# Performance work log

Measured on AMD Instinct MI355X. Metric: run time of the kernel, lower is better.

## Reference

```python
import jax, jax.numpy as jnp
import numpy as np

RADIUS = 4
SIGMA_X = 4.0
SIGMA_I = 10.0
P = 64                      # patch_size
NS = 2 * RADIUS + 1         # neighborhood_size = 9
EPS = float(np.finfo(np.float64).eps)


def _dist_weights():
    # Faithful to torch: dist varies only along the LAST window axis
    # (torch `expand` of a 1-D tensor to (9,9,9) broadcasts along dim -1).
    d = jnp.arange(1, NS + 1) - (RADIUS + 1)          # -4..4
    dist3d = jnp.broadcast_to(3 * d ** 2, (NS, NS, NS)).astype(jnp.float32)
    mask = (dist3d <= RADIUS).astype(jnp.float32)
    return (mask * jnp.exp(-dist3d / SIGMA_X ** 2)).reshape(-1)  # (729,)


_OFFSETS = jnp.asarray(
    np.stack(np.meshgrid(np.arange(NS), np.arange(NS), np.arange(NS), indexing='ij'),
             axis=-1).reshape(-1, 3), dtype=jnp.int32)            # (729, 3)


def _forward(batch, preds):
    B = batch.shape[0]
    K = preds.shape[1]
    pad = [(0, 0), (0, 0), (RADIUS, RADIUS), (RADIUS, RADIUS), (RADIUS, RADIUS)]
    pb = jnp.pad(batch, pad, constant_values=EPS)   # [B,1,P+2r,P+2r,P+2r]
    pp = jnp.pad(preds, pad, constant_values=EPS)   # [B,K,P+2r,P+2r,P+2r]
    dw = _dist_weights()

    def body(carry, od):
        off, w_o = od
        num, den = carry
        img_win = jax.lax.dynamic_slice(pb, (0, 0, off[0], off[1], off[2]),
                                        (B, 1, P, P, P))
        # Gaussian intensity affinity * spatial weight for this offset
        w = jnp.exp(-(img_win - batch) ** 2 / SIGMA_I ** 2) * w_o   # [B,1,P,P,P]
        pred_win = jax.lax.dynamic_slice(pp, (0, 0, off[0], off[1], off[2]),
                                         (B, K, P, P, P))
        return (num + w * pred_win, den + w), None

    num0 = jnp.zeros((B, K, P, P, P), batch.dtype)
    den0 = jnp.zeros((B, 1, P, P, P), batch.dtype)
    (num_map, den_map), _ = jax.lax.scan(body, (num0, den0), (_OFFSETS, dw))

    # Faithful to torch broadcasting: preds[B,1,P,P,P] * map[B,P,P,P] -> [B,B,...],
    # i.e. each sample's preds are contracted with the batch-summed maps.
    num_s = num_map.sum(axis=0)          # [K,P,P,P]
    den_s = den_map.sum(axis=0)[0]       # [P,P,P]
    numerator = jnp.einsum('bkxyz,kxyz->bk', preds, num_s)
    denominator = jnp.einsum('bkxyz,xyz->bk', preds, den_s)
    loss = (numerator + EPS) / (denominator + EPS)   # [B,K]
    return K - loss.sum(axis=1)                      # [B]


def setup_inputs() -> dict:
    key = jax.random.key(0)
    k1, k2 = jax.random.split(key)
    batch = jax.random.uniform(k1, (4, 1, P, P, P), dtype=jnp.float32)
    preds = jax.random.uniform(k2, (4, 4, P, P, P), dtype=jnp.float32)
    return {"batch": batch, "preds": preds}


def reference(batch, preds):
    return _forward(batch, preds)
```

## Files before the change

kernel.cpp:

```cpp
#include <hip/hip_runtime.h>
#include <hip/hip_fp16.h>


constexpr int Pdim = 64;
constexpr int P3   = Pdim * Pdim * Pdim;
constexpr int NREP = 16;

#define EPSF 2.2204460492503131e-16f

constexpr float WZ1   = 0.8290291181804004f;
constexpr float K2F   = 0.014426950408889634f;
constexpr float C1F   = 0.02f;
constexpr float WFULL = 81.0f * (1.0f + 2.0f * WZ1);

__global__ __launch_bounds__(256)
void ncuts_passx(const float* __restrict__ batch, const float* __restrict__ preds,
                 __half2* __restrict__ U, float* __restrict__ acc,
                 unsigned* __restrict__ ticket) {
  const int t = threadIdx.x;
  if (blockIdx.x == 0 && blockIdx.y == 0 && blockIdx.z == 0) {
    acc[t] = 0.f; acc[t + 256] = 0.f;
    if (t == 0) *ticket = 0u;
  }
  const int z = t & 63, yh = t >> 6;
  const int y = blockIdx.x * 4 + yh;
  const int pair = blockIdx.y;
  const int b = pair / 5, c = pair - 5 * b;
  const bool isden = (c == 4);
  const int X0 = 16 * (int)blockIdx.z - 4;
  const int lin = (y << 6) + z;
  const float* Ip = batch + b * P3 + lin;
  const float* Pp = isden ? Ip : preds + (b * 4 + c) * P3 + lin;
  __half2* Uo = U + pair * P3 + lin;

  float w0[9], w1[9];
#pragma unroll
  for (int i = 0; i < 9; ++i) { w0[i] = 0.f; w1[i] = 0.f; }
  float s0 = 0.f, s1 = 0.f;
#pragma unroll
  for (int i = 0; i < 24; ++i) {
    const int x = X0 + i;
    float u0 = 0.f, u1 = 0.f;
    if ((unsigned)x < 64u) {
      float I = Ip[x << 12];
      float g = exp2f(-I * I * K2F);
      float p = isden ? 1.f : Pp[x << 12];
      u0 = g * p;
      u1 = u0 * I;
    }
    const int r = i % 9;
    s0 += u0 - w0[r]; w0[r] = u0;
    s1 += u1 - w1[r]; w1[r] = u1;
    if (i >= 8) Uo[(x - 4) << 12] = __floats2half2_rn(s0, s1);
  }
}

__global__ __launch_bounds__(256)
void ncuts_passyz(const __half2* __restrict__ U, __half2* __restrict__ V) {
  const int t = threadIdx.x;
  const int z = t & 63, xh = t >> 6;
  const int x = blockIdx.x * 4 + xh;
  const int pair = blockIdx.y;
  const int Y0 = 16 * (int)blockIdx.z - 4;
  const __half2* src = U + pair * P3 + (x << 12) + z;
  __half2* dst = V + pair * P3 + (x << 12) + z;

  float w0[9], w1[9];
#pragma unroll
  for (int i = 0; i < 9; ++i) { w0[i] = 0.f; w1[i] = 0.f; }
  float s0 = 0.f, s1 = 0.f;
#pragma unroll
  for (int i = 0; i < 24; ++i) {
    const int y = Y0 + i;
    float u0 = 0.f, u1 = 0.f;
    if ((unsigned)y < 64u) {
      float2 u = __half22float2(src[y << 6]);
      u0 = u.x; u1 = u.y;
    }
    const int r = i % 9;
    s0 += u0 - w0[r]; w0[r] = u0;
    s1 += u1 - w1[r]; w1[r] = u1;
    if (i >= 8) {
      float up0 = __shfl_up(s0, 1, 64),   up1 = __shfl_up(s1, 1, 64);
      float dn0 = __shfl_down(s0, 1, 64), dn1 = __shfl_down(s1, 1, 64);
      if (z == 0)  { up0 = 0.f; up1 = 0.f; }
      if (z == 63) { dn0 = 0.f; dn1 = 0.f; }
      float v0 = __builtin_fmaf(WZ1, up0 + dn0, s0);
      float v1 = __builtin_fmaf(WZ1, up1 + dn1, s1);
      dst[(y - 4) << 6] = __floats2half2_rn(v0, v1);
    }
  }
}

__global__ __launch_bounds__(256)
void ncuts_contract(const float* __restrict__ batch, const float* __restrict__ preds,
                    const __half2* __restrict__ V, float* __restrict__ acc,
                    unsigned* __restrict__ ticket, float* __restrict__ out) {
  __shared__ float red[4][32];
  __shared__ int islast;
  const int t   = threadIdx.x;
  const int idx = blockIdx.x * 256 + t;
  const int v0  = idx << 1;
  const int z = v0 & 63, y = (v0 >> 6) & 63, x = v0 >> 12;

  float a0[4][2], a1[4][2], gsum[2] = {0.f, 0.f};
#pragma unroll
  for (int b = 0; b < 4; ++b) {
    float2 I = *(const float2*)(batch + b * P3 + v0);
    float g0 = exp2f(-I.x * I.x * K2F);
    float g1 = exp2f(-I.y * I.y * K2F);
    a0[b][0] = g0; a1[b][0] = g0 * I.x * C1F;
    a0[b][1] = g1; a1[b][1] = g1 * I.y * C1F;
    gsum[0] += g0; gsum[1] += g1;
  }

  float ns[4][2] = {{0.f,0.f},{0.f,0.f},{0.f,0.f},{0.f,0.f}};
  float ds[2] = {0.f, 0.f};
#pragma unroll
  for (int b = 0; b < 4; ++b) {
#pragma unroll
    for (int c = 0; c < 5; ++c) {
      float2 raw = *(const float2*)(V + (b * 5 + c) * P3 + v0);
      float2 u0 = __half22float2(__builtin_bit_cast(__half2, raw.x));
      float2 u1 = __half22float2(__builtin_bit_cast(__half2, raw.y));
      float zc0 = __builtin_fmaf(a0[b][0], u0.x, a1[b][0] * u0.y);
      float zc1 = __builtin_fmaf(a0[b][1], u1.x, a1[b][1] * u1.y);
      if (c < 4) { ns[c][0] += zc0; ns[c][1] += zc1; }
      else       { ds[0]    += zc0; ds[1]    += zc1; }
    }
  }
  float cx = 9.f - (float)max(0, 4 - x) - (float)max(0, x - 59);
  float cy = 9.f - (float)max(0, 4 - y) - (float)max(0, y - 59);
  float cz0 = 1.f + WZ1 * ((z > 0 ? 1.f : 0.f) + 1.f);
  float cz1 = 1.f + WZ1 * (1.f + (z + 1 < 63 ? 1.f : 0.f));
  ds[0] = __builtin_fmaf(gsum[0], WFULL - cx * cy * cz0, ds[0]);
  ds[1] = __builtin_fmaf(gsum[1], WFULL - cx * cy * cz1, ds[1]);

  float pn[16], pd[16];
#pragma unroll
  for (int b = 0; b < 4; ++b) {
#pragma unroll
    for (int k = 0; k < 4; ++k) {
      float2 p = *(const float2*)(preds + (b * 4 + k) * P3 + v0);
      pn[b * 4 + k] = p.x * ns[k][0] + p.y * ns[k][1];
      pd[b * 4 + k] = p.x * ds[0]    + p.y * ds[1];
    }
  }

#pragma unroll
  for (int i = 0; i < 16; ++i) {
#pragma unroll
    for (int off = 32; off > 0; off >>= 1) {
      pn[i] += __shfl_down(pn[i], off, 64);
      pd[i] += __shfl_down(pd[i], off, 64);
    }
  }
  const int wave = t >> 6, lane = t & 63;
  if (lane == 0) {
#pragma unroll
    for (int i = 0; i < 16; ++i) { red[wave][i] = pn[i]; red[wave][16 + i] = pd[i]; }
  }
  __syncthreads();
  if (t < 32) {
    float s = red[0][t] + red[1][t] + red[2][t] + red[3][t];
    atomicAdd(&acc[(blockIdx.x & (NREP - 1)) * 32 + t], s);
  }
  __syncthreads();
  if (t == 0) {
    unsigned done = atomicAdd(ticket, 1u);
    islast = (done == gridDim.x - 1);
  }
  __syncthreads();
  if (islast) {
    if (t < 32) {
      float n = 0.f;
      for (int r = 0; r < NREP; ++r) n += atomicAdd(&acc[r * 32 + t], 0.f);
      red[0][t] = n;
    }
    __syncthreads();
    if (t < 4) {
      float s = 0.f;
      for (int k = 0; k < 4; ++k)
        s += (red[0][t * 4 + k] + EPSF) / (red[0][16 + t * 4 + k] + EPSF);
      out[t] = 4.0f - s;
    }
  }
}

constexpr int Rxy = 4;
constexpr int TXf = 8, TYf = 8;
constexpr int ZLEN = 2;
constexpr int RGX = 16, RGY = 16, RGZ = 10;
constexpr int YPf = 17, ZPf = 11;

__global__ __launch_bounds__(256, 2)
void ncuts_mainf(const float* __restrict__ batch, const float* __restrict__ preds,
                 float* __restrict__ acc) {
  __shared__ float  sB[RGX][YPf][ZPf];
  __shared__ float4 sP[RGX][YPf][ZPf];
  __shared__ float  red[4][32];

  const int t = threadIdx.x;
  const int tx = t & 7, ty = (t >> 3) & 7, tzt = t >> 6;
  const int bx0 = blockIdx.x * TXf, by0 = blockIdx.y * TYf, bz0 = blockIdx.z * 8;
  const int x = bx0 + tx, y = by0 + ty, z0 = bz0 + tzt * ZLEN;
  const int zc = tzt * ZLEN;

  float  den[ZLEN];
  float4 num[ZLEN];
#pragma unroll
  for (int j = 0; j < ZLEN; ++j) { den[j] = 0.f; num[j] = make_float4(0.f, 0.f, 0.f, 0.f); }

  const float C1 = -0.014426950408889634f;
  const float LWZ1 = -0.27050531991668065f;

  for (int b = 0; b < 4; ++b) {
    __syncthreads();
    for (int idx = t; idx < RGX * RGY * RGZ; idx += 256) {
      int rz = idx % RGZ, rq = idx / RGZ, ry = rq % RGY, rx = rq / RGY;
      int gx = bx0 + rx - Rxy, gy = by0 + ry - Rxy, gz = bz0 + rz - 1;
      bool in = ((unsigned)gx < 64u) & ((unsigned)gy < 64u) & ((unsigned)gz < 64u);
      float v = EPSF; float4 pv = make_float4(EPSF, EPSF, EPSF, EPSF);
      if (in) {
        int gi = (gx * Pdim + gy) * Pdim + gz;
        v = batch[b * P3 + gi];
        const float* pp = preds + b * 4 * P3 + gi;
        pv.x = pp[0]; pv.y = pp[P3]; pv.z = pp[2 * P3]; pv.w = pp[3 * P3];
      }
      sB[rx][ry][rz] = v; sP[rx][ry][rz] = pv;
    }
    __syncthreads();

    float I0[ZLEN];
#pragma unroll
    for (int j = 0; j < ZLEN; ++j) I0[j] = sB[tx + Rxy][ty + Rxy][zc + 1 + j];

#pragma unroll 1
    for (int dy = 0; dy < 9; ++dy) {
#pragma unroll 3
      for (int dx = 0; dx < 9; ++dx) {
        const float*  cb = &sB[tx + dx][ty + dy][zc];
        const float4* cp = &sP[tx + dx][ty + dy][zc];
        float colB[ZLEN + 2]; float4 colP[ZLEN + 2];
#pragma unroll
        for (int j = 0; j < ZLEN + 2; ++j) { colB[j] = cb[j]; colP[j] = cp[j]; }
#pragma unroll
        for (int j = 0; j < ZLEN; ++j) {
#pragma unroll
          for (int dz = 0; dz < 3; ++dz) {
            float d = colB[j + dz] - I0[j];
            float arg = __builtin_fmaf(d * d, C1, (dz == 1) ? 0.f : LWZ1);
            float w = exp2f(arg);
            den[j] += w;
            float4 p = colP[j + dz];
            num[j].x = __builtin_fmaf(w, p.x, num[j].x);
            num[j].y = __builtin_fmaf(w, p.y, num[j].y);
            num[j].z = __builtin_fmaf(w, p.z, num[j].z);
            num[j].w = __builtin_fmaf(w, p.w, num[j].w);
          }
        }
      }
    }
  }

  float pn[16], pd[16];
#pragma unroll
  for (int i = 0; i < 16; ++i) { pn[i] = 0.f; pd[i] = 0.f; }
#pragma unroll
  for (int b = 0; b < 4; ++b) {
#pragma unroll
    for (int j = 0; j < ZLEN; ++j) {
      const float* pp = preds + b * 4 * P3 + ((x * Pdim + y) * Pdim + z0 + j);
      float nsv[4] = {num[j].x, num[j].y, num[j].z, num[j].w};
#pragma unroll
      for (int k = 0; k < 4; ++k) {
        float pv = pp[k * P3];
        pn[b * 4 + k] = __builtin_fmaf(pv, nsv[k], pn[b * 4 + k]);
        pd[b * 4 + k] = __builtin_fmaf(pv, den[j], pd[b * 4 + k]);
      }
    }
  }
#pragma unroll
  for (int i = 0; i < 16; ++i) {
#pragma unroll
    for (int off = 32; off > 0; off >>= 1) {
      pn[i] += __shfl_down(pn[i], off, 64);
      pd[i] += __shfl_down(pd[i], off, 64);
    }
  }
  const int wave = t >> 6, lane = t & 63;
  if (lane == 0) {
#pragma unroll
    for (int i = 0; i < 16; ++i) { red[wave][i] = pn[i]; red[wave][16 + i] = pd[i]; }
  }
  __syncthreads();
  if (t < 32) {
    float s = red[0][t] + red[1][t] + red[2][t] + red[3][t];
    int bid = blockIdx.x + 8 * (blockIdx.y + 8 * (int)blockIdx.z);
    atomicAdd(&acc[(bid & (NREP - 1)) * 32 + t], s);
  }
}

__global__ void ncuts_zero(float* __restrict__ acc) {
  int t = threadIdx.x;
  if (t < NREP * 32) acc[t] = 0.f;
}

__global__ void ncuts_final(const float* __restrict__ acc, float* __restrict__ out) {
  __shared__ float loss[16];
  int t = threadIdx.x;
  if (t < 16) {
    float n = 0.f, d = 0.f;
    for (int r = 0; r < NREP; ++r) { n += acc[r * 32 + t]; d += acc[r * 32 + 16 + t]; }
    loss[t] = (n + EPSF) / (d + EPSF);
  }
  __syncthreads();
  if (t < 4) {
    float s = loss[t * 4] + loss[t * 4 + 1] + loss[t * 4 + 2] + loss[t * 4 + 3];
    out[t] = 4.0f - s;
  }
}

extern "C" void kernel_launch(void* const* d_in, const int* in_sizes, int n_in,
                              void* d_out, int out_size, void* d_ws, size_t ws_size,
                              hipStream_t stream) {
  const float* batch = (const float*)d_in[0];
  const float* preds = (const float*)d_in[1];
  float* out = (float*)d_out;

  const size_t ub = (size_t)20 * P3 * sizeof(__half2);
  const size_t vb = ub;
  const size_t need = ub + vb + 8192;
  if (ws_size >= need) {
    char* base = (char*)d_ws;
    __half2*  U      = (__half2*)(base + 256);
    __half2*  V      = (__half2*)(base + 256 + ub);
    float*    acc    = (float*)(base + 512 + ub + vb);
    unsigned* ticket = (unsigned*)(base + 512 + ub + vb + 2048);
    hipLaunchKernelGGL(ncuts_passx, dim3(16, 20, 4), dim3(256), 0, stream,
                       batch, preds, U, acc, ticket);
    hipLaunchKernelGGL(ncuts_passyz, dim3(16, 20, 4), dim3(256), 0, stream, U, V);
    hipLaunchKernelGGL(ncuts_contract, dim3(512), dim3(256), 0, stream,
                       batch, preds, V, acc, ticket, out);
  } else {
    float* acc = (float*)d_ws;
    hipLaunchKernelGGL(ncuts_zero, dim3(1), dim3(512), 0, stream, acc);
    hipLaunchKernelGGL(ncuts_mainf, dim3(8, 8, 8), dim3(256), 0, stream,
                       batch, preds, acc);
    hipLaunchKernelGGL(ncuts_final, dim3(1), dim3(64), 0, stream, acc, out);
  }
}
```

Measured before the change: 102.2 us.

## Fuse y/z box-filter pass with contraction, dropping V intermediate buffer

Merges the y/z sliding-window pass and the contraction into one kernel. Each block handles one class channel across all four batch samples, keeps the filtered values in registers, and contracts them directly with preds, so the V buffer is never written or read back. The last-block ticket reduction is replaced by a separate small final kernel. The fused grid is much smaller (256 blocks) and each block loops serially over the batch, which may lower parallelism and latency hiding. The denominator U plane is also re-read once for every class channel.

```diff
diff --git a/kernel.cpp b/kernel.cpp
--- a/kernel.cpp
+++ b/kernel.cpp
@@ -15,12 +15,10 @@
 
 __global__ __launch_bounds__(256)
 void ncuts_passx(const float* __restrict__ batch, const float* __restrict__ preds,
-                 __half2* __restrict__ U, float* __restrict__ acc,
-                 unsigned* __restrict__ ticket) {
+                 __half2* __restrict__ U, float* __restrict__ acc) {
   const int t = threadIdx.x;
   if (blockIdx.x == 0 && blockIdx.y == 0 && blockIdx.z == 0) {
     acc[t] = 0.f; acc[t + 256] = 0.f;
-    if (t == 0) *ticket = 0u;
   }
   const int z = t & 63, yh = t >> 6;
   const int y = blockIdx.x * 4 + yh;
@@ -56,99 +54,84 @@
 }
 
 __global__ __launch_bounds__(256)
-void ncuts_passyz(const __half2* __restrict__ U, __half2* __restrict__ V) {
+void ncuts_fused(const float* __restrict__ batch, const float* __restrict__ preds,
+                 const __half2* __restrict__ U, float* __restrict__ acc) {
+  __shared__ float redn[4][4], redd[4][4];
   const int t = threadIdx.x;
   const int z = t & 63, xh = t >> 6;
   const int x = blockIdx.x * 4 + xh;
-  const int pair = blockIdx.y;
-  const int Y0 = 16 * (int)blockIdx.z - 4;
-  const __half2* src = U + pair * P3 + (x << 12) + z;
-  __half2* dst = V + pair * P3 + (x << 12) + z;
-
-  float w0[9], w1[9];
-#pragma unroll
-  for (int i = 0; i < 9; ++i) { w0[i] = 0.f; w1[i] = 0.f; }
-  float s0 = 0.f, s1 = 0.f;
-#pragma unroll
-  for (int i = 0; i < 24; ++i) {
-    const int y = Y0 + i;
-    float u0 = 0.f, u1 = 0.f;
-    if ((unsigned)y < 64u) {
-      float2 u = __half22float2(src[y << 6]);
-      u0 = u.x; u1 = u.y;
-    }
-    const int r = i % 9;
-    s0 += u0 - w0[r]; w0[r] = u0;
-    s1 += u1 - w1[r]; w1[r] = u1;
-    if (i >= 8) {
-      float up0 = __shfl_up(s0, 1, 64),   up1 = __shfl_up(s1, 1, 64);
-      float dn0 = __shfl_down(s0, 1, 64), dn1 = __shfl_down(s1, 1, 64);
-      if (z == 0)  { up0 = 0.f; up1 = 0.f; }
-      if (z == 63) { dn0 = 0.f; dn1 = 0.f; }
-      float v0 = __builtin_fmaf(WZ1, up0 + dn0, s0);
-      float v1 = __builtin_fmaf(WZ1, up1 + dn1, s1);
-      dst[(y - 4) << 6] = __floats2half2_rn(v0, v1);
-    }
-  }
-}
-
-__global__ __launch_bounds__(256)
-void ncuts_contract(const float* __restrict__ batch, const float* __restrict__ preds,
-                    const __half2* __restrict__ V, float* __restrict__ acc,
-                    unsigned* __restrict__ ticket, float* __restrict__ out) {
-  __shared__ float red[4][32];
-  __shared__ int islast;
-  const int t   = threadIdx.x;
-  const int idx = blockIdx.x * 256 + t;
-  const int v0  = idx << 1;
-  const int z = v0 & 63, y = (v0 >> 6) & 63, x = v0 >> 12;
-
-  float a0[4][2], a1[4][2], gsum[2] = {0.f, 0.f};
-#pragma unroll
+  const int c = blockIdx.y;
+  const int yo0 = 16 * (int)blockIdx.z;
+  const int Y0 = yo0 - 4;
+  const int xz = (x << 12) + z;
+
+  const float cx = 9.f - (float)max(0, 4 - x) - (float)max(0, x - 59);
+  const float cz = 1.f + WZ1 * ((z > 0 ? 1.f : 0.f) + (z < 63 ? 1.f : 0.f));
+
+  float Sc[16], S4[16];
+#pragma unroll
+  for (int j = 0; j < 16; ++j) { Sc[j] = 0.f; S4[j] = 0.f; }
+
+#pragma unroll 1
   for (int b = 0; b < 4; ++b) {
-    float2 I = *(const float2*)(batch + b * P3 + v0);
-    float g0 = exp2f(-I.x * I.x * K2F);
-    float g1 = exp2f(-I.y * I.y * K2F);
-    a0[b][0] = g0; a1[b][0] = g0 * I.x * C1F;
-    a0[b][1] = g1; a1[b][1] = g1 * I.y * C1F;
-    gsum[0] += g0; gsum[1] += g1;
-  }
-
-  float ns[4][2] = {{0.f,0.f},{0.f,0.f},{0.f,0.f},{0.f,0.f}};
-  float ds[2] = {0.f, 0.f};
-#pragma unroll
-  for (int b = 0; b < 4; ++b) {
-#pragma unroll
-    for (int c = 0; c < 5; ++c) {
-      float2 raw = *(const float2*)(V + (b * 5 + c) * P3 + v0);
-      float2 u0 = __half22float2(__builtin_bit_cast(__half2, raw.x));
-      float2 u1 = __half22float2(__builtin_bit_cast(__half2, raw.y));
-      float zc0 = __builtin_fmaf(a0[b][0], u0.x, a1[b][0] * u0.y);
-      float zc1 = __builtin_fmaf(a0[b][1], u1.x, a1[b][1] * u1.y);
-      if (c < 4) { ns[c][0] += zc0; ns[c][1] += zc1; }
-      else       { ds[0]    += zc0; ds[1]    += zc1; }
-    }
-  }
-  float cx = 9.f - (float)max(0, 4 - x) - (float)max(0, x - 59);
-  float cy = 9.f - (float)max(0, 4 - y) - (float)max(0, y - 59);
-  float cz0 = 1.f + WZ1 * ((z > 0 ? 1.f : 0.f) + 1.f);
-  float cz1 = 1.f + WZ1 * (1.f + (z + 1 < 63 ? 1.f : 0.f));
-  ds[0] = __builtin_fmaf(gsum[0], WFULL - cx * cy * cz0, ds[0]);
-  ds[1] = __builtin_fmaf(gsum[1], WFULL - cx * cy * cz1, ds[1]);
-
-  float pn[16], pd[16];
-#pragma unroll
-  for (int b = 0; b < 4; ++b) {
-#pragma unroll
-    for (int k = 0; k < 4; ++k) {
-      float2 p = *(const float2*)(preds + (b * 4 + k) * P3 + v0);
-      pn[b * 4 + k] = p.x * ns[k][0] + p.y * ns[k][1];
-      pd[b * 4 + k] = p.x * ds[0]    + p.y * ds[1];
-    }
-  }
-
-#pragma unroll
-  for (int i = 0; i < 16; ++i) {
+    const __half2* Un = U + (b * 5 + c) * P3 + xz;
+    const __half2* Ud = U + (b * 5 + 4) * P3 + xz;
+    const float*   Ip = batch + b * P3 + xz;
+    float nw0[9], nw1[9], dw0[9], dw1[9];
+#pragma unroll
+    for (int i = 0; i < 9; ++i) { nw0[i] = 0.f; nw1[i] = 0.f; dw0[i] = 0.f; dw1[i] = 0.f; }
+    float ns0 = 0.f, ns1 = 0.f, ds0 = 0.f, ds1 = 0.f;
+#pragma unroll
+    for (int i = 0; i < 24; ++i) {
+      const int y = Y0 + i;
+      float un0 = 0.f, un1 = 0.f, ud0 = 0.f, ud1 = 0.f;
+      if ((unsigned)y < 64u) {
+        float2 a = __half22float2(Un[y << 6]);
+        float2 d = __half22float2(Ud[y << 6]);
+        un0 = a.x; un1 = a.y; ud0 = d.x; ud1 = d.y;
+      }
+      const int r = i % 9;
+      ns0 += un0 - nw0[r]; nw0[r] = un0;
+      ns1 += un1 - nw1[r]; nw1[r] = un1;
+      ds0 += ud0 - dw0[r]; dw0[r] = ud0;
+      ds1 += ud1 - dw1[r]; dw1[r] = ud1;
+      if (i >= 8) {
+        const int yo = y - 4;
+        float a0 = __shfl_up(ns0, 1, 64),   a1 = __shfl_up(ns1, 1, 64);
+        float b0 = __shfl_down(ns0, 1, 64), b1 = __shfl_down(ns1, 1, 64);
+        float e0 = __shfl_up(ds0, 1, 64),   e1 = __shfl_up(ds1, 1, 64);
+        float f0 = __shfl_down(ds0, 1, 64), f1 = __shfl_down(ds1, 1, 64);
+        if (z == 0)  { a0 = 0.f; a1 = 0.f; e0 = 0.f; e1 = 0.f; }
+        if (z == 63) { b0 = 0.f; b1 = 0.f; f0 = 0.f; f1 = 0.f; }
+        float vn0 = __builtin_fmaf(WZ1, a0 + b0, ns0);
+        float vn1 = __builtin_fmaf(WZ1, a1 + b1, ns1);
+        float vd0 = __builtin_fmaf(WZ1, e0 + f0, ds0);
+        float vd1 = __builtin_fmaf(WZ1, e1 + f1, ds1);
+        float I  = Ip[yo << 6];
+        float g  = exp2f(-I * I * K2F);
+        float gi = g * I * C1F;
+        Sc[i - 8] += __builtin_fmaf(g, vn0, gi * vn1);
+        float cy = 9.f - (float)max(0, 4 - yo) - (float)max(0, yo - 59);
+        float corr = __builtin_fmaf(g, WFULL - cx * cy * cz, gi * vd1);
+        S4[i - 8] += __builtin_fmaf(g, vd0, corr);
+      }
+    }
+  }
+
+  float pn[4] = {0.f, 0.f, 0.f, 0.f}, pd[4] = {0.f, 0.f, 0.f, 0.f};
+#pragma unroll
+  for (int b2 = 0; b2 < 4; ++b2) {
+    const float* pp = preds + (b2 * 4 + c) * P3 + (x << 12) + (yo0 << 6) + z;
+#pragma unroll
+    for (int j = 0; j < 16; ++j) {
+      float p = pp[j << 6];
+      pn[b2] = __builtin_fmaf(p, Sc[j], pn[b2]);
+      pd[b2] = __builtin_fmaf(p, S4[j], pd[b2]);
+    }
+  }
+
+#pragma unroll
+  for (int i = 0; i < 4; ++i) {
 #pragma unroll
     for (int off = 32; off > 0; off >>= 1) {
       pn[i] += __shfl_down(pn[i], off, 64);
@@ -158,32 +141,30 @@
   const int wave = t >> 6, lane = t & 63;
   if (lane == 0) {
 #pragma unroll
-    for (int i = 0; i < 16; ++i) { red[wave][i] = pn[i]; red[wave][16 + i] = pd[i]; }
+    for (int i = 0; i < 4; ++i) { redn[wave][i] = pn[i]; redd[wave][i] = pd[i]; }
   }
   __syncthreads();
-  if (t < 32) {
-    float s = red[0][t] + red[1][t] + red[2][t] + red[3][t];
-    atomicAdd(&acc[(blockIdx.x & (NREP - 1)) * 32 + t], s);
+  if (t < 4) {
+    float n = redn[0][t] + redn[1][t] + redn[2][t] + redn[3][t];
+    float d = redd[0][t] + redd[1][t] + redd[2][t] + redd[3][t];
+    const int rep = ((int)blockIdx.x + 4 * (int)blockIdx.z) & (NREP - 1);
+    atomicAdd(&acc[rep * 32 + t * 4 + c], n);
+    atomicAdd(&acc[rep * 32 + 16 + t * 4 + c], d);
+  }
+}
+
+__global__ void ncuts_final(const float* __restrict__ acc, float* __restrict__ out) {
+  __shared__ float loss[16];
+  int t = threadIdx.x;
+  if (t < 16) {
+    float n = 0.f, d = 0.f;
+    for (int r = 0; r < NREP; ++r) { n += acc[r * 32 + t]; d += acc[r * 32 + 16 + t]; }
+    loss[t] = (n + EPSF) / (d + EPSF);
   }
   __syncthreads();
-  if (t == 0) {
-    unsigned done = atomicAdd(ticket, 1u);
-    islast = (done == gridDim.x - 1);
-  }
-  __syncthreads();
-  if (islast) {
-    if (t < 32) {
-      float n = 0.f;
-      for (int r = 0; r < NREP; ++r) n += atomicAdd(&acc[r * 32 + t], 0.f);
-      red[0][t] = n;
-    }
-    __syncthreads();
-    if (t < 4) {
-      float s = 0.f;
-      for (int k = 0; k < 4; ++k)
-        s += (red[0][t * 4 + k] + EPSF) / (red[0][16 + t * 4 + k] + EPSF);
-      out[t] = 4.0f - s;
-    }
+  if (t < 4) {
+    float s = loss[t * 4] + loss[t * 4 + 1] + loss[t * 4 + 2] + loss[t * 4 + 3];
+    out[t] = 4.0f - s;
   }
 }
 
@@ -306,21 +287,6 @@
   if (t < NREP * 32) acc[t] = 0.f;
 }
 
-__global__ void ncuts_final(const float* __restrict__ acc, float* __restrict__ out) {
-  __shared__ float loss[16];
-  int t = threadIdx.x;
-  if (t < 16) {
-    float n = 0.f, d = 0.f;
-    for (int r = 0; r < NREP; ++r) { n += acc[r * 32 + t]; d += acc[r * 32 + 16 + t]; }
-    loss[t] = (n + EPSF) / (d + EPSF);
-  }
-  __syncthreads();
-  if (t < 4) {
-    float s = loss[t * 4] + loss[t * 4 + 1] + loss[t * 4 + 2] + loss[t * 4 + 3];
-    out[t] = 4.0f - s;
-  }
-}
-
 extern "C" void kernel_launch(void* const* d_in, const int* in_sizes, int n_in,
                               void* d_out, int out_size, void* d_ws, size_t ws_size,
                               hipStream_t stream) {
@@ -329,19 +295,16 @@
   float* out = (float*)d_out;
 
   const size_t ub = (size_t)20 * P3 * sizeof(__half2);
-  const size_t vb = ub;
-  const size_t need = ub + vb + 8192;
+  const size_t need = ub + 8192;
   if (ws_size >= need) {
     char* base = (char*)d_ws;
-    __half2*  U      = (__half2*)(base + 256);
-    __half2*  V      = (__half2*)(base + 256 + ub);
-    float*    acc    = (float*)(base + 512 + ub + vb);
-    unsigned* ticket = (unsigned*)(base + 512 + ub + vb + 2048);
+    __half2* U   = (__half2*)(base + 256);
+    float*   acc = (float*)(base + 512 + ub);
     hipLaunchKernelGGL(ncuts_passx, dim3(16, 20, 4), dim3(256), 0, stream,
-                       batch, preds, U, acc, ticket);
-    hipLaunchKernelGGL(ncuts_passyz, dim3(16, 20, 4), dim3(256), 0, stream, U, V);
-    hipLaunchKernelGGL(ncuts_contract, dim3(512), dim3(256), 0, stream,
-                       batch, preds, V, acc, ticket, out);
+                       batch, preds, U, acc);
+    hipLaunchKernelGGL(ncuts_fused, dim3(16, 4, 4), dim3(256), 0, stream,
+                       batch, preds, U, acc);
+    hipLaunchKernelGGL(ncuts_final, dim3(1), dim3(64), 0, stream, acc, out);
   } else {
     float* acc = (float*)d_ws;
     hipLaunchKernelGGL(ncuts_zero, dim3(1), dim3(512), 0, stream, acc);
```

New measurement: 124.7 us. +22.0%, slower.
